# Kernel tuning notes

Measured on AMD Instinct MI355X. Metric: run time of the kernel, lower is better.

Reference implementation:

```python
import jax, jax.numpy as jnp
import numpy as np

N_QUERY = 100_000   # TotalQueryNodes
N_LATENT = 16_000   # TotalLatentNodes
K = 16              # neighbors per query (fixed-degree stand-in for radius graph)
C_IN = 64
C_OUT = 4
C_PROJ = 256
D = 3               # coord dim


def _glorot(key, shape):
    fan_in, fan_out = shape[0], shape[1]
    lim = np.sqrt(6.0 / (fan_in + fan_out))
    return jax.random.uniform(key, shape, jnp.float32, -lim, lim)


def setup_inputs() -> dict:
    key = jax.random.key(0)
    ks = jax.random.split(key, 16)
    rndata_flat = jax.random.normal(ks[0], (N_LATENT, C_IN), jnp.float32)
    phys_pos_query = jax.random.uniform(ks[1], (N_QUERY, D), jnp.float32)
    latent_tokens_pos = jax.random.uniform(ks[2], (N_LATENT, D), jnp.float32)
    batch_idx_phys_query = jnp.zeros((N_QUERY,), jnp.int64)
    latent_tokens_batch_idx = jnp.zeros((N_LATENT,), jnp.int64)
    # edge_index[0] = dst (query node), edge_index[1] = src (latent node)
    dst = jnp.repeat(jnp.arange(N_QUERY, dtype=jnp.int64), K)
    src = jax.random.randint(ks[3], (N_QUERY * K,), 0, N_LATENT).astype(jnp.int64)
    edge_index = jnp.stack([dst, src], axis=0)
    # kernel MLP: 2*D -> 64 -> 64 -> C_IN (GELU between layers, none after last)
    kW0 = _glorot(ks[4], (2 * D, 64)); kb0 = jnp.zeros((64,), jnp.float32)
    kW1 = _glorot(ks[5], (64, 64));    kb1 = jnp.zeros((64,), jnp.float32)
    kW2 = _glorot(ks[6], (64, C_IN)); kb2 = jnp.zeros((C_IN,), jnp.float32)
    # projection ChannelMLP: C_IN -> C_PROJ -> C_OUT
    pW1 = _glorot(ks[7], (C_IN, C_PROJ)); pb1 = jnp.zeros((C_PROJ,), jnp.float32)
    pW2 = _glorot(ks[8], (C_PROJ, C_OUT)); pb2 = jnp.zeros((C_OUT,), jnp.float32)
    return dict(rndata_flat=rndata_flat, phys_pos_query=phys_pos_query,
                batch_idx_phys_query=batch_idx_phys_query,
                latent_tokens_pos=latent_tokens_pos,
                latent_tokens_batch_idx=latent_tokens_batch_idx,
                edge_index=edge_index,
                kW0=kW0, kb0=kb0, kW1=kW1, kb1=kb1, kW2=kW2, kb2=kb2,
                pW1=pW1, pb1=pb1, pW2=pW2, pb2=pb2)


def reference(rndata_flat, phys_pos_query, batch_idx_phys_query,
              latent_tokens_pos, latent_tokens_batch_idx, edge_index,
              kW0, kb0, kW1, kb1, kW2, kb2, pW1, pb1, pW2, pb2):
    n_query = phys_pos_query.shape[0]
    dst = edge_index[0]  # query node per edge
    src = edge_index[1]  # latent node per edge
    gelu = lambda x: jax.nn.gelu(x, approximate=False)
    # IntegralTransform ('linear'): kernel MLP on concatenated coords per edge
    ef = jnp.concatenate([latent_tokens_pos[src], phys_pos_query[dst]], axis=-1)  # [E, 2D]
    h = gelu(ef @ kW0 + kb0)
    h = gelu(h @ kW1 + kb1)
    kern = h @ kW2 + kb2                      # [E, C_IN]
    rep = kern * rndata_flat[src]             # elementwise kernel * f_y  [E, C_IN]
    # mean-reduce over each query's neighborhood (scatter)
    num = jax.ops.segment_sum(rep, dst, num_segments=n_query)                 # [Nq, C_IN]
    cnt = jax.ops.segment_sum(jnp.ones((rep.shape[0], 1), rep.dtype), dst,
                              num_segments=n_query)
    decoded = num / jnp.maximum(cnt, 1.0)
    # single scale, no geoembed / scale weights -> final pointwise projection
    out = gelu(decoded @ pW1 + pb1) @ pW2 + pb2  # [Nq, C_OUT]
    return out
```

## Files before the change

kernel.cpp:

```cpp
#include <hip/hip_runtime.h>

typedef __attribute__((ext_vector_type(8))) __bf16 bf16x8;
typedef __attribute__((ext_vector_type(4))) float f32x4;
typedef __attribute__((ext_vector_type(4))) unsigned int u32x4;

union FragU { u32x4 u; bf16x8 b; };
union BfBits { __bf16 b; unsigned short s; };

#define MFMA16(A, B, C) __builtin_amdgcn_mfma_f32_16x16x32_bf16((A), (B), (C), 0, 0, 0)
#define SCHED_FENCE() __builtin_amdgcn_sched_barrier(0)

__device__ __forceinline__ float gelu_f(float x) {
    const float z = fabsf(x) * 0.70710678118654752440f;
    const float t = __builtin_amdgcn_rcpf(fmaf(0.3275911f, z, 1.0f));
    const float poly = t * (0.254829592f + t * (-0.284496736f + t * (1.421413741f +
                       t * (-1.453152027f + t * 1.061405429f))));
    const float e = 1.0f - poly * __expf(-z * z);
    const float s = copysignf(e, x);
    return 0.5f * x * (1.0f + s);
}

__device__ __forceinline__ void split8(const float x0, const float x1, const float x2,
                                       const float x3, const float x4, const float x5,
                                       const float x6, const float x7,
                                       bf16x8& hi, bf16x8& lo) {
    const float xs[8] = {x0, x1, x2, x3, x4, x5, x6, x7};
    FragU H, L;
    #pragma unroll
    for (int p = 0; p < 4; ++p) {
        const unsigned int h0m = (__float_as_uint(xs[2*p])   + 0x8000u) & 0xFFFF0000u;
        const unsigned int h1m = (__float_as_uint(xs[2*p+1]) + 0x8000u) & 0xFFFF0000u;
        H.u[p] = __builtin_amdgcn_perm(h1m, h0m, 0x07060302);
        const float r0 = xs[2*p]   - __uint_as_float(h0m);
        const float r1 = xs[2*p+1] - __uint_as_float(h1m);
        L.u[p] = __builtin_amdgcn_perm(__float_as_uint(r1), __float_as_uint(r0), 0x07060302);
    }
    hi = H.b; lo = L.b;
}

__global__ __launch_bounds__(256)
void prep_frags(const float* __restrict__ kW0, const float* __restrict__ kb0,
                const float* __restrict__ kW1, const float* __restrict__ kW2,
                const float* __restrict__ pW1,
                unsigned short* __restrict__ wsf)
{
    const int idx  = blockIdx.x * 256 + threadIdx.x;
    const int i    = idx & 7;
    const int lane = (idx >> 3) & 63;
    float val;
    int hl;
    if (idx < 4096) {
        const int rest = idx >> 9;
        hl = rest & 1;
        const int nt = rest >> 1;
        const int k = (lane >> 4) * 8 + i;
        const int n = nt * 16 + (lane & 15);
        val = (k < 6) ? kW0[k * 64 + n] : (k == 6 ? kb0[n] : 0.0f);
    } else if (idx < 12288) {
        const int rest = (idx - 4096) >> 9;
        hl = rest & 1;
        const int ntks = rest >> 1;
        const int nt = ntks & 3, ks = ntks >> 2;
        const int k = ks * 32 + (lane >> 4) * 8 + i;
        const int n = nt * 16 + (lane & 15);
        val = kW1[k * 64 + n];
    } else if (idx < 20480) {
        const int rest = (idx - 12288) >> 9;
        hl = rest & 1;
        const int ntks = rest >> 1;
        const int nt = ntks & 3, ks = ntks >> 2;
        const int k = ks * 32 + (lane >> 4) * 8 + i;
        const int n = nt * 16 + (lane & 15);
        val = kW2[k * 64 + n];
    } else {
        const int rest = (idx - 20480) >> 9;
        hl = rest & 1;
        const int ntks = rest >> 1;
        const int nt = ntks & 15, ks = ntks >> 4;
        const int k = ks * 32 + (lane >> 4) * 8 + i;
        const int n = nt * 16 + (lane & 15);
        val = pW1[k * 256 + n];
    }
    BfBits hi; hi.b = (__bf16)val;
    unsigned short ob;
    if (hl == 0) ob = hi.s;
    else { BfBits lo; lo.b = (__bf16)(val - (float)hi.b); ob = lo.s; }
    wsf[idx] = ob;
}

__global__ __launch_bounds__(256, 2)
void gno_mfma(const float* __restrict__ rndata,
              const float* __restrict__ qpos,
              const float* __restrict__ latpos,
              const int*   __restrict__ edge_src,
              const float* __restrict__ kb1, const float* __restrict__ kb2,
              const float* __restrict__ pb1,
              const float* __restrict__ pW2, const float* __restrict__ pb2,
              const unsigned short* __restrict__ wsf,
              float* __restrict__ out)
{
    __shared__ __align__(16) float sH[4][16][68];
    __shared__ __align__(16) float sdec[16][65];
    __shared__ float spart[4][16][4];
    __shared__ float sb1[64], sb2[64];

    const int tid = threadIdx.x;
    if (tid < 64) { sb1[tid] = kb1[tid]; sb2[tid] = kb2[tid]; }
    __syncthreads();

    const int l   = tid & 63;
    const int w   = tid >> 6;
    const int r15 = l & 15;
    const int g   = l >> 4;
    const int qbase = blockIdx.x * 16 + w * 4;

    const u32x4* wv = (const u32x4*)wsf;
    float (*myH)[68] = sH[w];

    #pragma unroll 1
    for (int t = 0; t < 4; ++t) {
        const int q = qbase + t;
        const int srcv = edge_src[q * 16 + r15];

        const float m0 = (g == 0) ? 1.0f : 0.0f;
        bf16x8 a0h, a0l;
        split8(latpos[srcv * 3 + 0] * m0, latpos[srcv * 3 + 1] * m0, latpos[srcv * 3 + 2] * m0,
               qpos[q * 3 + 0] * m0,      qpos[q * 3 + 1] * m0,      qpos[q * 3 + 2] * m0,
               m0, 0.0f, a0h, a0l);
        #pragma unroll
        for (int nt = 0; nt < 4; ++nt) {
            FragU wh, wl;
            wh.u = wv[(nt * 2 + 0) * 64 + l];
            wl.u = wv[(nt * 2 + 1) * 64 + l];
            f32x4 c = {0.f, 0.f, 0.f, 0.f};
            c = MFMA16(a0h, wh.b, c);
            c = MFMA16(a0l, wh.b, c);
            c = MFMA16(a0h, wl.b, c);
            #pragma unroll
            for (int j = 0; j < 4; ++j)
                myH[g * 4 + j][nt * 16 + r15] = gelu_f(c[j]);
        }
        SCHED_FENCE();

        bf16x8 a1h[2], a1l[2];
        #pragma unroll
        for (int ks = 0; ks < 2; ++ks) {
            const float* p = &myH[r15][ks * 32 + g * 8];
            const float4 xa = *(const float4*)p;
            const float4 xb = *(const float4*)(p + 4);
            split8(xa.x, xa.y, xa.z, xa.w, xb.x, xb.y, xb.z, xb.w, a1h[ks], a1l[ks]);
        }
        #pragma unroll
        for (int nt = 0; nt < 4; ++nt) {
            const float bv = sb1[nt * 16 + r15];
            f32x4 c = {bv, bv, bv, bv};
            #pragma unroll
            for (int ks = 0; ks < 2; ++ks) {
                FragU wh, wl;
                wh.u = wv[512 + ((ks * 4 + nt) * 2 + 0) * 64 + l];
                wl.u = wv[512 + ((ks * 4 + nt) * 2 + 1) * 64 + l];
                c = MFMA16(a1h[ks], wh.b, c);
                c = MFMA16(a1l[ks], wh.b, c);
                c = MFMA16(a1h[ks], wl.b, c);
            }
            #pragma unroll
            for (int j = 0; j < 4; ++j)
                myH[g * 4 + j][nt * 16 + r15] = gelu_f(c[j]);
        }
        SCHED_FENCE();

        bf16x8 a2h[2], a2l[2];
        #pragma unroll
        for (int ks = 0; ks < 2; ++ks) {
            const float* p = &myH[r15][ks * 32 + g * 8];
            const float4 xa = *(const float4*)p;
            const float4 xb = *(const float4*)(p + 4);
            split8(xa.x, xa.y, xa.z, xa.w, xb.x, xb.y, xb.z, xb.w, a2h[ks], a2l[ks]);
        }
        int se[4];
        #pragma unroll
        for (int r = 0; r < 4; ++r) se[r] = __shfl(srcv, g * 4 + r);
        #pragma unroll
        for (int nt = 0; nt < 4; ++nt) {
            const float bv = sb2[nt * 16 + r15];
            f32x4 c = {bv, bv, bv, bv};
            #pragma unroll
            for (int ks = 0; ks < 2; ++ks) {
                FragU wh, wl;
                wh.u = wv[1536 + ((ks * 4 + nt) * 2 + 0) * 64 + l];
                wl.u = wv[1536 + ((ks * 4 + nt) * 2 + 1) * 64 + l];
                c = MFMA16(a2h[ks], wh.b, c);
                c = MFMA16(a2l[ks], wh.b, c);
                c = MFMA16(a2h[ks], wl.b, c);
            }
            float v = 0.0f;
            #pragma unroll
            for (int r = 0; r < 4; ++r) {
                const float rnd = rndata[(size_t)se[r] * 64 + nt * 16 + r15];
                v += c[r] * rnd;
            }
            v += __shfl_xor(v, 16);
            v += __shfl_xor(v, 32);
            if (l < 16) sdec[w * 4 + t][nt * 16 + l] = v * 0.0625f;
        }
        SCHED_FENCE();
    }

    __syncthreads();

    bf16x8 pah[2], pal[2];
    #pragma unroll
    for (int ks = 0; ks < 2; ++ks) {
        const float* p = &sdec[r15][ks * 32 + g * 8];
        const float4 xa = *(const float4*)p;
        const float4 xb = *(const float4*)(p + 4);
        split8(xa.x, xa.y, xa.z, xa.w, xb.x, xb.y, xb.z, xb.w, pah[ks], pal[ks]);
    }

    float o[4][4];
    #pragma unroll
    for (int j = 0; j < 4; ++j)
        #pragma unroll
        for (int cc = 0; cc < 4; ++cc) o[j][cc] = 0.0f;

    #pragma unroll
    for (int ntl = 0; ntl < 4; ++ntl) {
        const int ntg = w * 4 + ntl;
        f32x4 c = {0.f, 0.f, 0.f, 0.f};
        #pragma unroll
        for (int ks = 0; ks < 2; ++ks) {
            FragU wh, wl;
            wh.u = wv[2560 + ((ks * 16 + ntg) * 2 + 0) * 64 + l];
            wl.u = wv[2560 + ((ks * 16 + ntg) * 2 + 1) * 64 + l];
            c = MFMA16(pah[ks], wh.b, c);
            c = MFMA16(pal[ks], wh.b, c);
            c = MFMA16(pah[ks], wl.b, c);
        }
        const int u = ntg * 16 + r15;
        const float bu = pb1[u];
        const float4 w2 = *(const float4*)&pW2[u * 4];
        #pragma unroll
        for (int j = 0; j < 4; ++j) {
            const float gv = gelu_f(c[j] + bu);
            o[j][0] += gv * w2.x; o[j][1] += gv * w2.y;
            o[j][2] += gv * w2.z; o[j][3] += gv * w2.w;
        }
    }
    #pragma unroll
    for (int j = 0; j < 4; ++j)
        #pragma unroll
        for (int cc = 0; cc < 4; ++cc) {
            o[j][cc] += __shfl_xor(o[j][cc], 1);
            o[j][cc] += __shfl_xor(o[j][cc], 2);
            o[j][cc] += __shfl_xor(o[j][cc], 4);
            o[j][cc] += __shfl_xor(o[j][cc], 8);
        }
    if (r15 == 0) {
        #pragma unroll
        for (int j = 0; j < 4; ++j)
            *(float4*)&spart[w][g * 4 + j][0] =
                make_float4(o[j][0], o[j][1], o[j][2], o[j][3]);
    }
    __syncthreads();

    if (tid < 64) {
        const int qq = tid >> 2, cc = tid & 3;
        const float val = spart[0][qq][cc] + spart[1][qq][cc]
                        + spart[2][qq][cc] + spart[3][qq][cc] + pb2[cc];
        out[(size_t)(blockIdx.x * 16 + qq) * 4 + cc] = val;
    }
}

extern "C" void kernel_launch(void* const* d_in, const int* in_sizes, int n_in,
                              void* d_out, int out_size, void* d_ws, size_t ws_size,
                              hipStream_t stream)
{
    const float* rndata = (const float*)d_in[0];
    const float* qpos   = (const float*)d_in[1];
    const float* latpos = (const float*)d_in[3];
    const int*   edge   = (const int*)d_in[5];
    const float* kW0 = (const float*)d_in[6];
    const float* kb0 = (const float*)d_in[7];
    const float* kW1 = (const float*)d_in[8];
    const float* kb1 = (const float*)d_in[9];
    const float* kW2 = (const float*)d_in[10];
    const float* kb2 = (const float*)d_in[11];
    const float* pW1 = (const float*)d_in[12];
    const float* pb1 = (const float*)d_in[13];
    const float* pW2 = (const float*)d_in[14];
    const float* pb2 = (const float*)d_in[15];
    float* out = (float*)d_out;

    const int E  = in_sizes[5] / 2;
    const int Nq = out_size / 4;

    prep_frags<<<208, 256, 0, stream>>>(kW0, kb0, kW1, kW2, pW1, (unsigned short*)d_ws);
    gno_mfma<<<Nq / 16, 256, 0, stream>>>(
        rndata, qpos, latpos, edge + E,
        kb1, kb2, pb1, pW2, pb2,
        (const unsigned short*)d_ws, out);
}
```

Measured before the change: 261.5 us.

## Stage MLP weight fragments in LDS and pre-split decoded values to bf16

Copies the layer-1 and layer-2 kernel-MLP weight fragments (32 KB) from global memory into shared memory once per block, so the per-query loops read them from LDS instead of global/L2. Biases move into registers. The decoded per-query values are split into bf16 hi/lo parts at write time and stored packed, so the projection stage reads ready-made MFMA fragments without re-splitting. The spart scratch is aliased onto sH to offset the added LDS use. The higher LDS footprint may reduce occupancy.

```diff
diff --git a/kernel.cpp b/kernel.cpp
--- a/kernel.cpp
+++ b/kernel.cpp
@@ -99,13 +99,16 @@
               const unsigned short* __restrict__ wsf,
               float* __restrict__ out)
 {
+    __shared__ __align__(16) u32x4 sWf[2048];
     __shared__ __align__(16) float sH[4][16][68];
-    __shared__ __align__(16) float sdec[16][65];
-    __shared__ float spart[4][16][4];
-    __shared__ float sb1[64], sb2[64];
+    __shared__ __align__(16) unsigned int sdech[16][32];
+    __shared__ __align__(16) unsigned int sdecl[16][32];
 
     const int tid = threadIdx.x;
-    if (tid < 64) { sb1[tid] = kb1[tid]; sb2[tid] = kb2[tid]; }
+    const u32x4* wv = (const u32x4*)wsf;
+
+    #pragma unroll
+    for (int i = 0; i < 8; ++i) sWf[i * 256 + tid] = wv[512 + i * 256 + tid];
     __syncthreads();
 
     const int l   = tid & 63;
@@ -114,7 +117,13 @@
     const int g   = l >> 4;
     const int qbase = blockIdx.x * 16 + w * 4;
 
-    const u32x4* wv = (const u32x4*)wsf;
+    float bv1[4], bv2[4];
+    #pragma unroll
+    for (int nt = 0; nt < 4; ++nt) {
+        bv1[nt] = kb1[nt * 16 + r15];
+        bv2[nt] = kb2[nt * 16 + r15];
+    }
+
     float (*myH)[68] = sH[w];
 
     #pragma unroll 1
@@ -152,13 +161,13 @@
         }
         #pragma unroll
         for (int nt = 0; nt < 4; ++nt) {
-            const float bv = sb1[nt * 16 + r15];
+            const float bv = bv1[nt];
             f32x4 c = {bv, bv, bv, bv};
             #pragma unroll
             for (int ks = 0; ks < 2; ++ks) {
                 FragU wh, wl;
-                wh.u = wv[512 + ((ks * 4 + nt) * 2 + 0) * 64 + l];
-                wl.u = wv[512 + ((ks * 4 + nt) * 2 + 1) * 64 + l];
+                wh.u = sWf[((ks * 4 + nt) * 2 + 0) * 64 + l];
+                wl.u = sWf[((ks * 4 + nt) * 2 + 1) * 64 + l];
                 c = MFMA16(a1h[ks], wh.b, c);
                 c = MFMA16(a1l[ks], wh.b, c);
                 c = MFMA16(a1h[ks], wl.b, c);
@@ -182,13 +191,13 @@
         for (int r = 0; r < 4; ++r) se[r] = __shfl(srcv, g * 4 + r);
         #pragma unroll
         for (int nt = 0; nt < 4; ++nt) {
-            const float bv = sb2[nt * 16 + r15];
+            const float bv = bv2[nt];
             f32x4 c = {bv, bv, bv, bv};
             #pragma unroll
             for (int ks = 0; ks < 2; ++ks) {
                 FragU wh, wl;
-                wh.u = wv[1536 + ((ks * 4 + nt) * 2 + 0) * 64 + l];
-                wl.u = wv[1536 + ((ks * 4 + nt) * 2 + 1) * 64 + l];
+                wh.u = sWf[1024 + ((ks * 4 + nt) * 2 + 0) * 64 + l];
+                wl.u = sWf[1024 + ((ks * 4 + nt) * 2 + 1) * 64 + l];
                 c = MFMA16(a2h[ks], wh.b, c);
                 c = MFMA16(a2l[ks], wh.b, c);
                 c = MFMA16(a2h[ks], wl.b, c);
@@ -201,20 +210,31 @@
             }
             v += __shfl_xor(v, 16);
             v += __shfl_xor(v, 32);
-            if (l < 16) sdec[w * 4 + t][nt * 16 + l] = v * 0.0625f;
+            const float s = v * 0.0625f;
+            const unsigned int sm = (__float_as_uint(s) + 0x8000u) & 0xFFFF0000u;
+            const float sr = s - __uint_as_float(sm);
+            const unsigned int smn = __shfl_xor(sm, 1);
+            const float srn = __shfl_xor(sr, 1);
+            if (l < 16 && (l & 1) == 0) {
+                sdech[w * 4 + t][nt * 8 + (l >> 1)] =
+                    __builtin_amdgcn_perm(smn, sm, 0x07060302);
+                sdecl[w * 4 + t][nt * 8 + (l >> 1)] =
+                    __builtin_amdgcn_perm(__float_as_uint(srn), __float_as_uint(sr), 0x07060302);
+            }
         }
         SCHED_FENCE();
     }
 
     __syncthreads();
+    float (*spart)[16][4] = (float (*)[16][4])&sH[0][0][0];
 
     bf16x8 pah[2], pal[2];
     #pragma unroll
     for (int ks = 0; ks < 2; ++ks) {
-        const float* p = &sdec[r15][ks * 32 + g * 8];
-        const float4 xa = *(const float4*)p;
-        const float4 xb = *(const float4*)(p + 4);
-        split8(xa.x, xa.y, xa.z, xa.w, xb.x, xb.y, xb.z, xb.w, pah[ks], pal[ks]);
+        FragU PH, PL;
+        PH.u = *(const u32x4*)&sdech[r15][ks * 16 + g * 4];
+        PL.u = *(const u32x4*)&sdecl[r15][ks * 16 + g * 4];
+        pah[ks] = PH.b; pal[ks] = PL.b;
     }
 
     float o[4][4];
```

New measurement: 270.2 us. +3.3%, slower.
